# Kernel optimization log

Measured on AMD Instinct MI355X. Metric: run time of the kernel, lower is better.

## Reference

```python
import jax, jax.numpy as jnp
import numpy as np

K = 1024  # attention hidden dim
H = 1024  # encoder hidden dim


def setup_inputs() -> dict:
    key = jax.random.key(0)
    ks = jax.random.split(key, 8)
    B, S = 32, 2048
    decoder_state = jax.random.normal(ks[0], (B, H), dtype=jnp.float32)
    encoder_hiddens = jax.random.normal(ks[1], (B, S, H), dtype=jnp.float32)
    # Linear params (torch convention: y = x @ W.T + b)
    Wa_w = jax.random.normal(ks[2], (1, K), dtype=jnp.float32) / np.sqrt(K)
    Wa_b = jnp.zeros((1,), dtype=jnp.float32)
    Wb_w = jax.random.normal(ks[3], (K, H), dtype=jnp.float32) / np.sqrt(H)
    Wb_b = jnp.zeros((K,), dtype=jnp.float32)
    Wc_w = jax.random.normal(ks[4], (K, H), dtype=jnp.float32) / np.sqrt(H)
    Wc_b = jnp.zeros((K,), dtype=jnp.float32)
    return {
        "decoder_state": decoder_state,
        "encoder_hiddens": encoder_hiddens,
        "Wa_w": Wa_w, "Wa_b": Wa_b,
        "Wb_w": Wb_w, "Wb_b": Wb_b,
        "Wc_w": Wc_w, "Wc_b": Wc_b,
    }


def reference(decoder_state, encoder_hiddens, Wa_w, Wa_b, Wb_w, Wb_b, Wc_w, Wc_b):
    # dec_proj: [B, K]; enc_proj: [B, S, K]
    dec_proj = decoder_state @ Wb_w.T + Wb_b
    enc_proj = jnp.einsum('bsh,kh->bsk', encoder_hiddens, Wc_w) + Wc_b
    # additive score: tanh then project to scalar -> [B, S]
    e = jnp.tanh(dec_proj[:, None, :] + enc_proj)
    scores = jnp.einsum('bsk,k->bs', e, Wa_w[0]) + Wa_b[0]
    attn = jax.nn.softmax(scores, axis=1)
    # weighted sum over sequence -> [B, H]
    context = jnp.einsum('bs,bsh->bh', attn, encoder_hiddens)
    return context
```

## Files before the change

kernel.cpp:

```cpp
#include <hip/hip_runtime.h>
#include <hip/hip_bf16.h>
#include <stdint.h>

#define B_SZ 32
#define S_SZ 2048
#define H_SZ 1024
#define K_SZ 1024
#define M_SZ (B_SZ * S_SZ)

typedef __attribute__((ext_vector_type(8))) short bf16x8;
typedef __attribute__((ext_vector_type(4))) float f32x4;


__device__ __forceinline__ short f2bf_rne(float f) {
    uint32_t u = __builtin_bit_cast(uint32_t, f);
    u += 0x7fffu + ((u >> 16) & 1u);
    return (short)(u >> 16);
}

__device__ __forceinline__ float bf2f(unsigned short u) {
    return __builtin_bit_cast(float, (uint32_t)u << 16);
}

__device__ __forceinline__ float fast_tanh(float x) {
    float ex = __expf(2.0f * x);
    return 1.0f - 2.0f / (ex + 1.0f);
}


__global__ void cvt_bf16_k(const float* __restrict__ in,
                           __hip_bfloat16* __restrict__ out, int n8) {
    int idx = blockIdx.x * blockDim.x + threadIdx.x;
    int stride = gridDim.x * blockDim.x;
    for (int i = idx; i < n8; i += stride) {
        const float4* p = (const float4*)in + (size_t)i * 2;
        float4 a = p[0], b = p[1];
        bf16x8 r;
        r[0] = f2bf_rne(a.x); r[1] = f2bf_rne(a.y);
        r[2] = f2bf_rne(a.z); r[3] = f2bf_rne(a.w);
        r[4] = f2bf_rne(b.x); r[5] = f2bf_rne(b.y);
        r[6] = f2bf_rne(b.z); r[7] = f2bf_rne(b.w);
        ((bf16x8*)out)[i] = r;
    }
}


__global__ __launch_bounds__(256) void decproj_k(
    const float* __restrict__ ds, const float* __restrict__ Wb,
    const float* __restrict__ Wb_b, const float* __restrict__ Wc_b,
    float* __restrict__ dp) {
    int g = blockIdx.x * 4 + (threadIdx.x >> 6);
    int lane = threadIdx.x & 63;
    int b = g >> 10;
    int k = g & 1023;
    const float4* wrow = (const float4*)(Wb + (size_t)k * H_SZ);
    const float4* xrow = (const float4*)(ds + (size_t)b * H_SZ);
    float sum = 0.f;
#pragma unroll
    for (int it = 0; it < 4; it++) {
        float4 w = wrow[lane + it * 64];
        float4 x = xrow[lane + it * 64];
        sum += w.x * x.x + w.y * x.y + w.z * x.z + w.w * x.w;
    }
#pragma unroll
    for (int off = 1; off < 64; off <<= 1) sum += __shfl_xor(sum, off, 64);
    if (lane == 0) dp[g] = sum + Wb_b[k] + Wc_b[k];
}


__device__ __forceinline__ void stage2(const __hip_bfloat16* __restrict__ srcRowBase,
                                       unsigned char* ldsHt, int k0,
                                       size_t laneOff, int ldsLane) {
#pragma unroll
    for (int inst = 0; inst < 2; inst++) {
        const char* g = (const char*)srcRowBase + (size_t)k0 * 2 + laneOff +
                        (size_t)inst * (64 * H_SZ * 2);
        __builtin_amdgcn_global_load_lds(
            (const __attribute__((address_space(1))) void*)g,
            (__attribute__((address_space(3))) void*)(ldsHt + inst * 8192 + ldsLane),
            16, 0, 0);
    }
}

__device__ __forceinline__ void read_afr(bf16x8 (&afr)[2][2], const unsigned char* Abuf,
                                         int aRowB, int phOff, int kOff0, int kOff1) {
#pragma unroll
    for (int i = 0; i < 2; ++i) {
        afr[i][0] = *(const bf16x8*)(Abuf + aRowB + phOff + i * 2048 + kOff0);
        afr[i][1] = *(const bf16x8*)(Abuf + aRowB + phOff + i * 2048 + kOff1);
    }
}

__device__ __forceinline__ void read_bfr(bf16x8 (&bfr)[4][2], const unsigned char* Bbuf,
                                         int bRowB, int kOff0, int kOff1) {
#pragma unroll
    for (int n = 0; n < 4; ++n) {
        bfr[n][0] = *(const bf16x8*)(Bbuf + bRowB + n * 2048 + kOff0);
        bfr[n][1] = *(const bf16x8*)(Bbuf + bRowB + n * 2048 + kOff1);
    }
}

template <int VM, bool SA, bool SB>
__device__ __forceinline__ void tile_run(
    const __hip_bfloat16* __restrict__ AgR, const __hip_bfloat16* __restrict__ BgR,
    const unsigned char* Acur, unsigned char* BcurW, unsigned char* Anxt,
    int kA, int kB, size_t laneOff, int ldsLane,
    int aRowB, int bRowB, int kOff0, int kOff1,
    f32x4 (&acc)[8][4])
{
    bf16x8 bfr[4][2];
#pragma unroll
    for (int ph = 0; ph < 4; ++ph) {
        if (ph == 0) read_bfr(bfr, BcurW, bRowB, kOff0, kOff1);
        bf16x8 afr[2][2];
        read_afr(afr, Acur, aRowB, ph * 4096, kOff0, kOff1);
        if (SA && ph == 0) stage2(AgR,                Anxt,          kA, laneOff, ldsLane);
        if (SA && ph == 1) stage2(AgR + 128 * H_SZ,   Anxt + 16384,  kA, laneOff, ldsLane);
        if (SB && ph == 2) stage2(BgR,                BcurW,         kB, laneOff, ldsLane);
        if (SB && ph == 3) stage2(BgR + 128 * H_SZ,   BcurW + 16384, kB, laneOff, ldsLane);
        __builtin_amdgcn_s_barrier();
        asm volatile("s_waitcnt lgkmcnt(0)" ::: "memory");
        __builtin_amdgcn_s_setprio(1);
#pragma unroll
        for (int i = 0; i < 2; ++i)
#pragma unroll
            for (int ks = 0; ks < 2; ++ks)
#pragma unroll
                for (int n = 0; n < 4; ++n)
                    acc[ph * 2 + i][n] = __builtin_amdgcn_mfma_f32_16x16x32_bf16(
                        afr[i][ks], bfr[n][ks], acc[ph * 2 + i][n], 0, 0, 0);
        __builtin_amdgcn_s_setprio(0);
        if (ph == 3 && VM == 4) asm volatile("s_waitcnt vmcnt(4)" ::: "memory");
        if (ph == 3 && VM == 0) asm volatile("s_waitcnt vmcnt(0)" ::: "memory");
        __builtin_amdgcn_s_barrier();
    }
}

__global__ __launch_bounds__(512, 2) void gemm256_scores_k(
    const __hip_bfloat16* __restrict__ Ag, const __hip_bfloat16* __restrict__ Bg,
    const float* __restrict__ decp, const float* __restrict__ Wa,
    float* __restrict__ sp)
{
    __shared__ __align__(16) unsigned char lds[131072];
    const int t = threadIdx.x;
    const int wave = t >> 6, lane = t & 63;
    const int wr = wave >> 2, wc = wave & 3;
    const int quad = lane >> 4, l15 = lane & 15;

    const int id = blockIdx.x;
    const int colBlk = (id >> 3) & 3;
    const int rowBlk = ((id >> 5) << 3) | (id & 7);
    const int row0 = rowBlk * 256, col0 = colBlk * 256;

    const int swz = (l15 & 7) << 4;
    const int aRowB = (wr * 128 + l15) * 128;
    const int bRowB = (wc * 64 + l15) * 128;
    const int kOff0 = (quad * 16) ^ swz;
    const int kOff1 = (64 + quad * 16) ^ swz;

    const size_t laneOff = (size_t)(t >> 3) * (H_SZ * 2) +
                           ((((t & 7) ^ ((t >> 3) & 7)) << 4));
    const int ldsLane = (t >> 6) << 10;
    const __hip_bfloat16* AgR = Ag + (size_t)row0 * H_SZ;
    const __hip_bfloat16* BgR = Bg + (size_t)col0 * H_SZ;

    f32x4 acc[8][4];
#pragma unroll
    for (int i = 0; i < 8; i++)
#pragma unroll
        for (int j = 0; j < 4; j++) acc[i][j] = f32x4{0.f, 0.f, 0.f, 0.f};

    unsigned char* A0l = lds;
    unsigned char* B0l = lds + 32768;
    unsigned char* A1l = lds + 65536;
    unsigned char* B1l = lds + 98304;

    stage2(BgR,                B0l,          0, laneOff, ldsLane);
    stage2(BgR + 128 * H_SZ,   B0l + 16384,  0, laneOff, ldsLane);
    stage2(AgR,                A0l,          0, laneOff, ldsLane);
    stage2(AgR + 128 * H_SZ,   A0l + 16384,  0, laneOff, ldsLane);
    stage2(BgR,                B1l,         64, laneOff, ldsLane);
    stage2(BgR + 128 * H_SZ,   B1l + 16384, 64, laneOff, ldsLane);
    asm volatile("s_waitcnt vmcnt(4)" ::: "memory");
    __builtin_amdgcn_s_barrier();

#pragma unroll 2
    for (int tt = 0; tt < 14; ++tt) {
        unsigned char* Ac = (tt & 1) ? A1l : A0l;
        unsigned char* Bc = (tt & 1) ? B1l : B0l;
        unsigned char* An = (tt & 1) ? A0l : A1l;
        tile_run<4, true, true>(AgR, BgR, Ac, Bc, An,
                                (tt + 1) * 64, (tt + 2) * 64, laneOff, ldsLane,
                                aRowB, bRowB, kOff0, kOff1, acc);
    }
    tile_run<0, true, false>(AgR, BgR, A0l, B0l, A1l,
                             15 * 64, 0, laneOff, ldsLane,
                             aRowB, bRowB, kOff0, kOff1, acc);
    tile_run<-1, false, false>(AgR, BgR, A1l, B1l, A0l,
                               0, 0, laneOff, ldsLane,
                               aRowB, bRowB, kOff0, kOff1, acc);

    const int b = row0 >> 11;
    float wa_j[4], dp_j[4];
#pragma unroll
    for (int n = 0; n < 4; ++n) {
        int c = col0 + wc * 64 + n * 16 + l15;
        wa_j[n] = Wa[c];
        dp_j[n] = decp[b * K_SZ + c];
    }
    const int slotIdx = colBlk * 4 + wc;
#pragma unroll
    for (int m = 0; m < 8; ++m) {
#pragma unroll
        for (int r = 0; r < 4; ++r) {
            float tsum = 0.f;
#pragma unroll
            for (int n = 0; n < 4; ++n)
                tsum += wa_j[n] * fast_tanh(acc[m][n][r] + dp_j[n]);
#pragma unroll
            for (int off = 1; off < 16; off <<= 1) tsum += __shfl_xor(tsum, off, 64);
            if (l15 == 0) {
                int mrow = row0 + wr * 128 + m * 16 + quad * 4 + r;
                sp[(size_t)slotIdx * M_SZ + mrow] = tsum;
            }
        }
    }
}


template <bool AF32>
__global__ __launch_bounds__(256) void gemm_scores_k(
    const void* __restrict__ Aptr, const __hip_bfloat16* __restrict__ Bw,
    const float* __restrict__ decp, const float* __restrict__ Wa,
    float* __restrict__ sp) {
    constexpr int ABYTES = AF32 ? 128 * 32 * 4 : 128 * 32 * 2;
    __shared__ __align__(16) unsigned char AsmRaw[ABYTES];
    __shared__ __align__(16) unsigned char BsmRaw[128 * 32 * 2];

    const int t = threadIdx.x;
    const int wave = t >> 6;
    const int lane = t & 63;
    const int wm = wave >> 1, wn = wave & 1;
    const int quad = lane >> 4;
    const int l15 = lane & 15;

    const int id = blockIdx.x;
    const int colBlk = (id >> 3) & 7;
    const int rowBlk = ((id >> 6) << 3) | (id & 7);
    const int row0 = rowBlk * 128;
    const int col0 = colBlk * 128;
    const int b = row0 >> 11;

    f32x4 acc[4][4];
#pragma unroll
    for (int i = 0; i < 4; i++)
#pragma unroll
        for (int j = 0; j < 4; j++) acc[i][j] = f32x4{0.f, 0.f, 0.f, 0.f};

    const __hip_bfloat16* Ab = (const __hip_bfloat16*)Aptr;
    const float* Af = (const float*)Aptr;

    for (int k0 = 0; k0 < H_SZ; k0 += 32) {
        if constexpr (AF32) {
#pragma unroll
            for (int inst = 0; inst < 4; inst++) {
                int slot = inst * 256 + t;
                int r = slot >> 3, c4 = slot & 7;
                const float* g = Af + (size_t)(row0 + r) * H_SZ + k0 + c4 * 4;
                __builtin_amdgcn_global_load_lds(
                    (const __attribute__((address_space(1))) void*)g,
                    (__attribute__((address_space(3))) void*)(AsmRaw + inst * 4096 + wave * 1024),
                    16, 0, 0);
            }
        } else {
#pragma unroll
            for (int inst = 0; inst < 2; inst++) {
                int slot = inst * 256 + t;
                int r = slot >> 2, c8 = slot & 3;
                const __hip_bfloat16* g = Ab + (size_t)(row0 + r) * H_SZ + k0 + c8 * 8;
                __builtin_amdgcn_global_load_lds(
                    (const __attribute__((address_space(1))) void*)g,
                    (__attribute__((address_space(3))) void*)(AsmRaw + inst * 4096 + wave * 1024),
                    16, 0, 0);
            }
        }
#pragma unroll
        for (int inst = 0; inst < 2; inst++) {
            int slot = inst * 256 + t;
            int r = slot >> 2, c8 = slot & 3;
            const __hip_bfloat16* g = Bw + (size_t)(col0 + r) * H_SZ + k0 + c8 * 8;
            __builtin_amdgcn_global_load_lds(
                (const __attribute__((address_space(1))) void*)g,
                (__attribute__((address_space(3))) void*)(BsmRaw + inst * 4096 + wave * 1024),
                16, 0, 0);
        }
        __syncthreads();

        bf16x8 afr[4], bfr[4];
#pragma unroll
        for (int i = 0; i < 4; i++) {
            int r = wm * 64 + i * 16 + l15;
            if constexpr (AF32) {
                const float* ap = (const float*)AsmRaw + r * 32 + quad * 8;
                f32x4 lo = *(const f32x4*)ap;
                f32x4 hi = *(const f32x4*)(ap + 4);
                bf16x8 v;
                v[0] = f2bf_rne(lo[0]); v[1] = f2bf_rne(lo[1]);
                v[2] = f2bf_rne(lo[2]); v[3] = f2bf_rne(lo[3]);
                v[4] = f2bf_rne(hi[0]); v[5] = f2bf_rne(hi[1]);
                v[6] = f2bf_rne(hi[2]); v[7] = f2bf_rne(hi[3]);
                afr[i] = v;
            } else {
                afr[i] = *(const bf16x8*)((const __hip_bfloat16*)AsmRaw + r * 32 + quad * 8);
            }
        }
#pragma unroll
        for (int j = 0; j < 4; j++) {
            int r = wn * 64 + j * 16 + l15;
            bfr[j] = *(const bf16x8*)((const __hip_bfloat16*)BsmRaw + r * 32 + quad * 8);
        }
#pragma unroll
        for (int i = 0; i < 4; i++)
#pragma unroll
            for (int j = 0; j < 4; j++)
                acc[i][j] = __builtin_amdgcn_mfma_f32_16x16x32_bf16(afr[i], bfr[j], acc[i][j], 0, 0, 0);
        __syncthreads();
    }

    float wa_j[4], dp_j[4];
#pragma unroll
    for (int j = 0; j < 4; j++) {
        int c = col0 + wn * 64 + j * 16 + l15;
        wa_j[j] = Wa[c];
        dp_j[j] = decp[b * K_SZ + c];
    }
    const int slotIdx = colBlk * 2 + wn;
#pragma unroll
    for (int i = 0; i < 4; i++) {
#pragma unroll
        for (int r = 0; r < 4; r++) {
            float tsum = 0.f;
#pragma unroll
            for (int j = 0; j < 4; j++)
                tsum += wa_j[j] * fast_tanh(acc[i][j][r] + dp_j[j]);
#pragma unroll
            for (int off = 1; off < 16; off <<= 1) tsum += __shfl_xor(tsum, off, 64);
            if (l15 == 0) {
                int m = row0 + wm * 64 + i * 16 + quad * 4 + r;
                sp[(size_t)slotIdx * M_SZ + m] = tsum;
            }
        }
    }
}


__global__ __launch_bounds__(256) void softmax_k(
    const float* __restrict__ sp, float* __restrict__ attn) {
    int b = blockIdx.x;
    int t = threadIdx.x;
    __shared__ float wred[4];
    __shared__ float wred2[4];
    float sc[8];
    float mx = -1e30f;
#pragma unroll
    for (int u = 0; u < 8; u++) {
        int m = b * S_SZ + t + u * 256;
        float v = 0.f;
#pragma unroll
        for (int c = 0; c < 16; c++) v += sp[(size_t)c * M_SZ + m];
        sc[u] = v;
        mx = fmaxf(mx, v);
    }
#pragma unroll
    for (int off = 1; off < 64; off <<= 1) mx = fmaxf(mx, __shfl_xor(mx, off, 64));
    if ((t & 63) == 0) wred[t >> 6] = mx;
    __syncthreads();
    mx = fmaxf(fmaxf(wred[0], wred[1]), fmaxf(wred[2], wred[3]));
    float lsum = 0.f;
#pragma unroll
    for (int u = 0; u < 8; u++) { sc[u] = expf(sc[u] - mx); lsum += sc[u]; }
#pragma unroll
    for (int off = 1; off < 64; off <<= 1) lsum += __shfl_xor(lsum, off, 64);
    if ((t & 63) == 0) wred2[t >> 6] = lsum;
    __syncthreads();
    float inv = 1.f / (wred2[0] + wred2[1] + wred2[2] + wred2[3]);
#pragma unroll
    for (int u = 0; u < 8; u++) attn[b * S_SZ + t + u * 256] = sc[u] * inv;
}


template <bool BF16E>
__global__ __launch_bounds__(256) void ctx_part_k(
    const float* __restrict__ attn, const void* __restrict__ encp,
    float* __restrict__ cp) {
    int b = blockIdx.x >> 5;
    int c = blockIdx.x & 31;
    int t = threadIdx.x;
    __shared__ float wloc[64];
    if (t < 64) wloc[t] = attn[b * S_SZ + c * 64 + t];
    __syncthreads();
    float4 acc = {0.f, 0.f, 0.f, 0.f};
    if constexpr (BF16E) {
        const ushort4* ep = (const ushort4*)((const __hip_bfloat16*)encp +
                              ((size_t)b * S_SZ + (size_t)c * 64) * H_SZ);
#pragma unroll 8
        for (int s = 0; s < 64; s++) {
            float w = wloc[s];
            ushort4 v = ep[s * 256 + t];
            acc.x += w * bf2f(v.x); acc.y += w * bf2f(v.y);
            acc.z += w * bf2f(v.z); acc.w += w * bf2f(v.w);
        }
    } else {
        const float4* ep = (const float4*)((const float*)encp +
                              ((size_t)b * S_SZ + (size_t)c * 64) * H_SZ);
#pragma unroll 8
        for (int s = 0; s < 64; s++) {
            float w = wloc[s];
            float4 v = ep[s * 256 + t];
            acc.x += w * v.x; acc.y += w * v.y;
            acc.z += w * v.z; acc.w += w * v.w;
        }
    }
    ((float4*)(cp + ((size_t)c * B_SZ + b) * H_SZ))[t] = acc;
}

__global__ void ctx_red_k(const float* __restrict__ cp, float* __restrict__ out) {
    int i = blockIdx.x * blockDim.x + threadIdx.x;
    float s = 0.f;
#pragma unroll
    for (int c = 0; c < 32; c++) s += cp[(size_t)c * (B_SZ * H_SZ) + i];
    out[i] = s;
}


extern "C" void kernel_launch(void* const* d_in, const int* in_sizes, int n_in,
                              void* d_out, int out_size, void* d_ws, size_t ws_size,
                              hipStream_t stream) {
    const float* dec  = (const float*)d_in[0];
    const float* enc  = (const float*)d_in[1];
    const float* Wa_w = (const float*)d_in[2];
    const float* Wb_w = (const float*)d_in[4];
    const float* Wb_b = (const float*)d_in[5];
    const float* Wc_w = (const float*)d_in[6];
    const float* Wc_b = (const float*)d_in[7];
    float* out = (float*)d_out;

    char* ws = (char*)d_ws;
    size_t off = 0;
    auto alloc = [&](size_t bytes) -> void* {
        void* p = ws + off;
        off += (bytes + 255) & ~(size_t)255;
        return p;
    };
    __hip_bfloat16* wc_bf = (__hip_bfloat16*)alloc((size_t)K_SZ * H_SZ * 2);
    float* dp     = (float*)alloc((size_t)B_SZ * K_SZ * 4);
    float* spart  = (float*)alloc((size_t)16 * M_SZ * 4);
    float* attn   = (float*)alloc((size_t)B_SZ * S_SZ * 4);
    float* cpart  = (float*)alloc((size_t)32 * B_SZ * H_SZ * 4);
    __hip_bfloat16* enc_bf = (__hip_bfloat16*)alloc((size_t)M_SZ * H_SZ * 2);
    const bool useBf16A = (off <= ws_size);

    cvt_bf16_k<<<512, 256, 0, stream>>>(Wc_w, wc_bf, K_SZ * H_SZ / 8);
    if (useBf16A)
        cvt_bf16_k<<<8192, 256, 0, stream>>>(enc, enc_bf, M_SZ * H_SZ / 8);
    decproj_k<<<8192, 256, 0, stream>>>(dec, Wb_w, Wb_b, Wc_b, dp);
    if (useBf16A)
        gemm256_scores_k<<<(M_SZ / 256) * (K_SZ / 256), 512, 0, stream>>>(enc_bf, wc_bf, dp, Wa_w, spart);
    else
        gemm_scores_k<true><<<(M_SZ / 128) * 8, 256, 0, stream>>>(enc, wc_bf, dp, Wa_w, spart);
    softmax_k<<<B_SZ, 256, 0, stream>>>(spart, attn);
    if (useBf16A)
        ctx_part_k<true><<<B_SZ * 32, 256, 0, stream>>>(attn, enc_bf, cpart);
    else
        ctx_part_k<false><<<B_SZ * 32, 256, 0, stream>>>(attn, enc, cpart);
    ctx_red_k<<<128, 256, 0, stream>>>(cpart, out);
}
```

Measured before the change: 579.1 us.

## Fuse preprocessing kernels, halve GEMM barriers, replace context reduction with atomics

Merges the Wc and encoder bf16 conversions and the decoder projection into one launch that also zeroes the output. The GEMM inner tile drops from four barrier pairs per k-step to two, grouping two MFMA phases between each barrier. The context step now atomically adds partial sums into the output, removing the partial buffer and its reduction kernel. The intent is to cut launch overhead and synchronisation stalls. In exchange, atomics make float summation order nondeterministic, and the looser barriers must still protect the LDS buffers that stage2 overwrites.

```diff
diff --git a/kernel.cpp b/kernel.cpp
--- a/kernel.cpp
+++ b/kernel.cpp
@@ -28,43 +28,58 @@
 }
 
 
-__global__ void cvt_bf16_k(const float* __restrict__ in,
-                           __hip_bfloat16* __restrict__ out, int n8) {
-    int idx = blockIdx.x * blockDim.x + threadIdx.x;
-    int stride = gridDim.x * blockDim.x;
-    for (int i = idx; i < n8; i += stride) {
-        const float4* p = (const float4*)in + (size_t)i * 2;
+__global__ __launch_bounds__(256) void fused_pre_k(
+    const float* __restrict__ Wc, __hip_bfloat16* __restrict__ wc_bf,
+    const float* __restrict__ enc, __hip_bfloat16* __restrict__ enc_bf,
+    int encB,
+    const float* __restrict__ ds, const float* __restrict__ Wb,
+    const float* __restrict__ Wb_b, const float* __restrict__ Wc_b,
+    float* __restrict__ dp, float* __restrict__ out)
+{
+    const int blk = blockIdx.x;
+    const int t = threadIdx.x;
+    if (blk < 512) {
+        int i = blk * 256 + t;
+        const float4* p = (const float4*)Wc + (size_t)i * 2;
         float4 a = p[0], b = p[1];
         bf16x8 r;
         r[0] = f2bf_rne(a.x); r[1] = f2bf_rne(a.y);
         r[2] = f2bf_rne(a.z); r[3] = f2bf_rne(a.w);
         r[4] = f2bf_rne(b.x); r[5] = f2bf_rne(b.y);
         r[6] = f2bf_rne(b.z); r[7] = f2bf_rne(b.w);
-        ((bf16x8*)out)[i] = r;
-    }
-}
-
-
-__global__ __launch_bounds__(256) void decproj_k(
-    const float* __restrict__ ds, const float* __restrict__ Wb,
-    const float* __restrict__ Wb_b, const float* __restrict__ Wc_b,
-    float* __restrict__ dp) {
-    int g = blockIdx.x * 4 + (threadIdx.x >> 6);
-    int lane = threadIdx.x & 63;
-    int b = g >> 10;
-    int k = g & 1023;
-    const float4* wrow = (const float4*)(Wb + (size_t)k * H_SZ);
-    const float4* xrow = (const float4*)(ds + (size_t)b * H_SZ);
-    float sum = 0.f;
-#pragma unroll
-    for (int it = 0; it < 4; it++) {
-        float4 w = wrow[lane + it * 64];
-        float4 x = xrow[lane + it * 64];
-        sum += w.x * x.x + w.y * x.y + w.z * x.z + w.w * x.w;
-    }
-#pragma unroll
-    for (int off = 1; off < 64; off <<= 1) sum += __shfl_xor(sum, off, 64);
-    if (lane == 0) dp[g] = sum + Wb_b[k] + Wc_b[k];
+        ((bf16x8*)wc_bf)[i] = r;
+        if (blk < 32) ((float4*)out)[blk * 256 + t] = float4{0.f, 0.f, 0.f, 0.f};
+    } else if (blk < 512 + encB) {
+        int idx = (blk - 512) * 256 + t;
+        int stride = encB * 256;
+        for (int i = idx; i < M_SZ * H_SZ / 8; i += stride) {
+            const float4* p = (const float4*)enc + (size_t)i * 2;
+            float4 a = p[0], b = p[1];
+            bf16x8 r;
+            r[0] = f2bf_rne(a.x); r[1] = f2bf_rne(a.y);
+            r[2] = f2bf_rne(a.z); r[3] = f2bf_rne(a.w);
+            r[4] = f2bf_rne(b.x); r[5] = f2bf_rne(b.y);
+            r[6] = f2bf_rne(b.z); r[7] = f2bf_rne(b.w);
+            ((bf16x8*)enc_bf)[i] = r;
+        }
+    } else {
+        int g = (blk - 512 - encB) * 4 + (t >> 6);
+        int lane = t & 63;
+        int b = g >> 10;
+        int k = g & 1023;
+        const float4* wrow = (const float4*)(Wb + (size_t)k * H_SZ);
+        const float4* xrow = (const float4*)(ds + (size_t)b * H_SZ);
+        float sum = 0.f;
+#pragma unroll
+        for (int it = 0; it < 4; it++) {
+            float4 w = wrow[lane + it * 64];
+            float4 x = xrow[lane + it * 64];
+            sum += w.x * x.x + w.y * x.y + w.z * x.z + w.w * x.w;
+        }
+#pragma unroll
+        for (int off = 1; off < 64; off <<= 1) sum += __shfl_xor(sum, off, 64);
+        if (lane == 0) dp[g] = sum + Wb_b[k] + Wc_b[k];
+    }
 }
 
 
@@ -98,6 +113,20 @@
         bfr[n][0] = *(const bf16x8*)(Bbuf + bRowB + n * 2048 + kOff0);
         bfr[n][1] = *(const bf16x8*)(Bbuf + bRowB + n * 2048 + kOff1);
     }
+}
+
+__device__ __forceinline__ void mfma_ph(f32x4 (&acc)[8][4], const bf16x8 (&afr)[2][2],
+                                        const bf16x8 (&bfr)[4][2], int base) {
+    __builtin_amdgcn_s_setprio(1);
+#pragma unroll
+    for (int i = 0; i < 2; ++i)
+#pragma unroll
+        for (int ks = 0; ks < 2; ++ks)
+#pragma unroll
+            for (int n = 0; n < 4; ++n)
+                acc[base + i][n] = __builtin_amdgcn_mfma_f32_16x16x32_bf16(
+                    afr[i][ks], bfr[n][ks], acc[base + i][n], 0, 0, 0);
+    __builtin_amdgcn_s_setprio(0);
 }
 
 template <int VM, bool SA, bool SB>
@@ -109,31 +138,37 @@
     f32x4 (&acc)[8][4])
 {
     bf16x8 bfr[4][2];
-#pragma unroll
-    for (int ph = 0; ph < 4; ++ph) {
-        if (ph == 0) read_bfr(bfr, BcurW, bRowB, kOff0, kOff1);
+    read_bfr(bfr, BcurW, bRowB, kOff0, kOff1);
+    {
         bf16x8 afr[2][2];
-        read_afr(afr, Acur, aRowB, ph * 4096, kOff0, kOff1);
-        if (SA && ph == 0) stage2(AgR,                Anxt,          kA, laneOff, ldsLane);
-        if (SA && ph == 1) stage2(AgR + 128 * H_SZ,   Anxt + 16384,  kA, laneOff, ldsLane);
-        if (SB && ph == 2) stage2(BgR,                BcurW,         kB, laneOff, ldsLane);
-        if (SB && ph == 3) stage2(BgR + 128 * H_SZ,   BcurW + 16384, kB, laneOff, ldsLane);
-        __builtin_amdgcn_s_barrier();
-        asm volatile("s_waitcnt lgkmcnt(0)" ::: "memory");
-        __builtin_amdgcn_s_setprio(1);
-#pragma unroll
-        for (int i = 0; i < 2; ++i)
-#pragma unroll
-            for (int ks = 0; ks < 2; ++ks)
-#pragma unroll
-                for (int n = 0; n < 4; ++n)
-                    acc[ph * 2 + i][n] = __builtin_amdgcn_mfma_f32_16x16x32_bf16(
-                        afr[i][ks], bfr[n][ks], acc[ph * 2 + i][n], 0, 0, 0);
-        __builtin_amdgcn_s_setprio(0);
-        if (ph == 3 && VM == 4) asm volatile("s_waitcnt vmcnt(4)" ::: "memory");
-        if (ph == 3 && VM == 0) asm volatile("s_waitcnt vmcnt(0)" ::: "memory");
-        __builtin_amdgcn_s_barrier();
-    }
+        read_afr(afr, Acur, aRowB, 0, kOff0, kOff1);
+        if (SA) stage2(AgR, Anxt, kA, laneOff, ldsLane);
+        mfma_ph(acc, afr, bfr, 0);
+    }
+    {
+        bf16x8 afr[2][2];
+        read_afr(afr, Acur, aRowB, 4096, kOff0, kOff1);
+        if (SA) stage2(AgR + 128 * H_SZ, Anxt + 16384, kA, laneOff, ldsLane);
+        mfma_ph(acc, afr, bfr, 2);
+    }
+    asm volatile("s_waitcnt lgkmcnt(0)" ::: "memory");
+    __builtin_amdgcn_s_barrier();
+    {
+        bf16x8 afr[2][2];
+        read_afr(afr, Acur, aRowB, 8192, kOff0, kOff1);
+        if (SB) stage2(BgR, BcurW, kB, laneOff, ldsLane);
+        mfma_ph(acc, afr, bfr, 4);
+    }
+    {
+        bf16x8 afr[2][2];
+        read_afr(afr, Acur, aRowB, 12288, kOff0, kOff1);
+        if (SB) stage2(BgR + 128 * H_SZ, BcurW + 16384, kB, laneOff, ldsLane);
+        mfma_ph(acc, afr, bfr, 6);
+    }
+    if (VM == 4) asm volatile("s_waitcnt vmcnt(4)" ::: "memory");
+    if (VM == 0) asm volatile("s_waitcnt vmcnt(0)" ::: "memory");
+    asm volatile("s_waitcnt lgkmcnt(0)" ::: "memory");
+    __builtin_amdgcn_s_barrier();
 }
 
 __global__ __launch_bounds__(512, 2) void gemm256_scores_k(
@@ -389,9 +424,35 @@
 }
 
 
-template <bool BF16E>
+__global__ __launch_bounds__(256) void ctx_atomic_k(
+    const float* __restrict__ attn, const __hip_bfloat16* __restrict__ encp,
+    float* __restrict__ out) {
+    int b = blockIdx.x >> 5;
+    int c = blockIdx.x & 31;
+    int t = threadIdx.x;
+    __shared__ float wloc[64];
+    if (t < 64) wloc[t] = attn[b * S_SZ + c * 64 + t];
+    __syncthreads();
+    float4 acc = {0.f, 0.f, 0.f, 0.f};
+    const ushort4* ep = (const ushort4*)(encp +
+                          ((size_t)b * S_SZ + (size_t)c * 64) * H_SZ);
+#pragma unroll 8
+    for (int s = 0; s < 64; s++) {
+        float w = wloc[s];
+        ushort4 v = ep[s * 256 + t];
+        acc.x += w * bf2f(v.x); acc.y += w * bf2f(v.y);
+        acc.z += w * bf2f(v.z); acc.w += w * bf2f(v.w);
+    }
+    float* o = out + (size_t)b * H_SZ + t * 4;
+    atomicAdd(o + 0, acc.x);
+    atomicAdd(o + 1, acc.y);
+    atomicAdd(o + 2, acc.z);
+    atomicAdd(o + 3, acc.w);
+}
+
+
 __global__ __launch_bounds__(256) void ctx_part_k(
-    const float* __restrict__ attn, const void* __restrict__ encp,
+    const float* __restrict__ attn, const float* __restrict__ encp,
     float* __restrict__ cp) {
     int b = blockIdx.x >> 5;
     int c = blockIdx.x & 31;
@@ -400,26 +461,14 @@
     if (t < 64) wloc[t] = attn[b * S_SZ + c * 64 + t];
     __syncthreads();
     float4 acc = {0.f, 0.f, 0.f, 0.f};
-    if constexpr (BF16E) {
-        const ushort4* ep = (const ushort4*)((const __hip_bfloat16*)encp +
-                              ((size_t)b * S_SZ + (size_t)c * 64) * H_SZ);
+    const float4* ep = (const float4*)(encp +
+                          ((size_t)b * S_SZ + (size_t)c * 64) * H_SZ);
 #pragma unroll 8
-        for (int s = 0; s < 64; s++) {
-            float w = wloc[s];
-            ushort4 v = ep[s * 256 + t];
-            acc.x += w * bf2f(v.x); acc.y += w * bf2f(v.y);
-            acc.z += w * bf2f(v.z); acc.w += w * bf2f(v.w);
-        }
-    } else {
-        const float4* ep = (const float4*)((const float*)encp +
-                              ((size_t)b * S_SZ + (size_t)c * 64) * H_SZ);
-#pragma unroll 8
-        for (int s = 0; s < 64; s++) {
-            float w = wloc[s];
-            float4 v = ep[s * 256 + t];
-            acc.x += w * v.x; acc.y += w * v.y;
-            acc.z += w * v.z; acc.w += w * v.w;
-        }
+    for (int s = 0; s < 64; s++) {
+        float w = wloc[s];
+        float4 v = ep[s * 256 + t];
+        acc.x += w * v.x; acc.y += w * v.y;
+        acc.z += w * v.z; acc.w += w * v.w;
     }
     ((float4*)(cp + ((size_t)c * B_SZ + b) * H_SZ))[t] = acc;
 }
@@ -460,18 +509,18 @@
     __hip_bfloat16* enc_bf = (__hip_bfloat16*)alloc((size_t)M_SZ * H_SZ * 2);
     const bool useBf16A = (off <= ws_size);
 
-    cvt_bf16_k<<<512, 256, 0, stream>>>(Wc_w, wc_bf, K_SZ * H_SZ / 8);
-    if (useBf16A)
-        cvt_bf16_k<<<8192, 256, 0, stream>>>(enc, enc_bf, M_SZ * H_SZ / 8);
-    decproj_k<<<8192, 256, 0, stream>>>(dec, Wb_w, Wb_b, Wc_b, dp);
+    const int encB = useBf16A ? 8192 : 0;
+    fused_pre_k<<<512 + encB + 8192, 256, 0, stream>>>(
+        Wc_w, wc_bf, enc, enc_bf, encB, dec, Wb_w, Wb_b, Wc_b, dp, out);
     if (useBf16A)
         gemm256_scores_k<<<(M_SZ / 256) * (K_SZ / 256), 512, 0, stream>>>(enc_bf, wc_bf, dp, Wa_w, spart);
     else
         gemm_scores_k<true><<<(M_SZ / 128) * 8, 256, 0, stream>>>(enc, wc_bf, dp, Wa_w, spart);
     softmax_k<<<B_SZ, 256, 0, stream>>>(spart, attn);
-    if (useBf16A)
-        ctx_part_k<true><<<B_SZ * 32, 256, 0, stream>>>(attn, enc_bf, cpart);
-    else
-        ctx_part_k<false><<<B_SZ * 32, 256, 0, stream>>>(attn, enc, cpart);
-    ctx_red_k<<<128, 256, 0, stream>>>(cpart, out);
-}
+    if (useBf16A) {
+        ctx_atomic_k<<<B_SZ * 32, 256, 0, stream>>>(attn, enc_bf, out);
+    } else {
+        ctx_part_k<<<B_SZ * 32, 256, 0, stream>>>(attn, enc, cpart);
+        ctx_red_k<<<128, 256, 0, stream>>>(cpart, out);
+    }
+}
```

After: 565.7 us. 1.02x faster.
